# Kernel tuning notes

Hardware: AMD Instinct MI355X
Metric: run time of the kernel (lower is better)

## Reference

```python
import jax, jax.numpy as jnp
import numpy as np

H_S = 4
W_S = 4


def setup_inputs() -> dict:
    key = jax.random.key(0)
    k1, k2 = jax.random.split(key)
    x1 = jax.random.normal(k1, (8, 128, 96, 320), dtype=jnp.float32)
    x2 = jax.random.normal(k2, (8, 128, 96, 320), dtype=jnp.float32)
    return {"x1": x1, "x2": x2}


def reference(x1, x2):
    # torch F.pad p2d=(h_s,h_s,w_s,w_s) pads last dim (W) by h_s and H by w_s
    b, c, h, w = x1.shape
    padded = jnp.pad(x2, ((0, 0), (0, 0), (W_S, W_S), (H_S, H_S)))
    costs = []
    for y in range(2 * H_S + 1):
        for x in range(2 * W_S + 1):
            sl = padded[:, :, y:y + h, x:x + w]  # [B,C,H,W]
            costs.append(jnp.mean(x1 * sl, axis=1))  # [B,H,W]
    cost_vol = jnp.stack(costs, axis=1)  # [B,81,H,W]
    return jax.nn.leaky_relu(cost_vol, negative_slope=0.1)
```

## Files before the change

### kernel.cpp

```cpp
#include <hip/hip_runtime.h>
#include <stdint.h>


#define CCH   128
#define HH    96
#define WW    320
#define HWs   (HH * WW)
#define CHWs  (CCH * HWs)
#define ND    81

#define TH 4
#define WT 32
#define SW 40
#define SR 12
#define KC 32
#define KP 40
#define OP 132

typedef __attribute__((ext_vector_type(8))) short        short8;
typedef __attribute__((ext_vector_type(4))) float        floatx4;
typedef __attribute__((ext_vector_type(4))) unsigned int uint4v;

__device__ __forceinline__ unsigned int bf16rne(float f) {
  unsigned int u = __float_as_uint(f);
  return (u + 0x7fffu + ((u >> 16) & 1u)) >> 16;
}
__device__ __forceinline__ unsigned int pk2(float lo, float hi) {
  return bf16rne(lo) | (bf16rne(hi) << 16);
}

__global__ __launch_bounds__(512, 4) void cost_volume_kernel(
    const float* __restrict__ x1g, const float* __restrict__ x2g,
    float* __restrict__ out)
{
  extern __shared__ char smem[];
  short* x2s  = (short*)smem;
  float* obuf = (float*)smem;

  const int b  = blockIdx.x & 7;
  const int g  = blockIdx.x >> 3;
  const int hs = g % 24;
  const int ws = g / 24;
  const int h0 = hs * TH;
  const int W0 = ws * WT;

  const int t    = threadIdx.x;
  const int wave = t >> 6;
  const int lane = t & 63;
  const int hl   = wave >> 1;
  const int mt   = wave & 1;
  const int q    = lane >> 4;
  const int ln   = lane & 15;

  const float* x1b = x1g + (size_t)b * CHWs;
  const float* x2b = x2g + (size_t)b * CHWs;

  int x2_go[4], x2_lo[4];
#pragma unroll
  for (int s = 0; s < 4; ++s) {
    int u = t + s * 512;
    if (u < SR * SW * 4) {
      int j  = u % SW;
      int ro = u / SW;
      int o  = ro & 3;
      int r  = ro >> 2;
      int gr = h0 - 4 + r;
      int gc = W0 - 4 + j;
      x2_lo[s] = (r * SW + j) * KP + o * 8;
      x2_go[s] = (gr >= 0 && gr < HH && gc >= 0 && gc < WW)
                   ? (o * 8 * HWs + gr * WW + gc) : -1;
    } else { x2_lo[s] = -1; x2_go[s] = -1; }
  }
  const int x1off = (h0 + hl) * WW + W0 + mt * 16 + ln;

  floatx4 acc[9][2] = {};

  for (int kc = 0; kc < CCH / KC; ++kc) {
    const int cbase = kc * KC * HWs;

    const float* p1 = x1b + cbase + (size_t)q * 8 * HWs + x1off;
    float a0 = p1[0 * HWs], a1 = p1[1 * HWs], a2 = p1[2 * HWs], a3 = p1[3 * HWs];
    float a4 = p1[4 * HWs], a5 = p1[5 * HWs], a6 = p1[6 * HWs], a7 = p1[7 * HWs];

#pragma unroll
    for (int s = 0; s < 4; ++s) {
      if (x2_lo[s] >= 0) {
        unsigned int p01 = 0, p23 = 0, p45 = 0, p67 = 0;
        if (x2_go[s] >= 0) {
          const float* p = x2b + cbase + x2_go[s];
          float f0 = p[0 * HWs], f1 = p[1 * HWs], f2 = p[2 * HWs], f3 = p[3 * HWs];
          float f4 = p[4 * HWs], f5 = p[5 * HWs], f6 = p[6 * HWs], f7 = p[7 * HWs];
          p01 = pk2(f0, f1); p23 = pk2(f2, f3);
          p45 = pk2(f4, f5); p67 = pk2(f6, f7);
        }
        *(uint4v*)&x2s[x2_lo[s]] = (uint4v){p01, p23, p45, p67};
      }
    }

    short8 af;
    {
      uint4v av = (uint4v){pk2(a0, a1), pk2(a2, a3), pk2(a4, a5), pk2(a6, a7)};
      af = *(short8*)&av;
    }
    __syncthreads();

#pragma unroll
    for (int dyi = 0; dyi < 9; ++dyi) {
      const int r = hl + dyi;
#pragma unroll
      for (int jn = 0; jn < 2; ++jn) {
        int jc = (mt + jn) * 16 + ln;
        if (jc > SW - 1) jc = SW - 1;
        const short8 bf = *(const short8*)&x2s[(r * SW + jc) * KP + q * 8];
        acc[dyi][jn] = __builtin_amdgcn_mfma_f32_16x16x32_bf16(af, bf, acc[dyi][jn], 0, 0, 0);
      }
    }
    __syncthreads();
  }

  const size_t obase = (size_t)b * (ND * (size_t)HWs);
#pragma unroll
  for (int ph = 0; ph < 2; ++ph) {
    const int d0 = ph ? 5 : 0, d1 = ph ? 9 : 5;
#pragma unroll
    for (int dyi = 0; dyi < 9; ++dyi) {
      if (dyi < d0 || dyi >= d1) continue;
#pragma unroll
      for (int jn = 0; jn < 2; ++jn)
#pragma unroll
        for (int reg = 0; reg < 4; ++reg) {
          const int m   = q * 4 + reg;
          const int dxi = jn * 16 + ln - m;
          if (dxi >= 0 && dxi < 9) {
            float v = acc[dyi][jn][reg] * (1.0f / 128.0f);
            v = (v < 0.0f) ? 0.1f * v : v;
            obuf[((dyi - d0) * 9 + dxi) * OP + hl * WT + mt * 16 + m] = v;
          }
        }
    }
    __syncthreads();
    const int nd   = (d1 - d0) * 9;
    const int dbas = d0 * 9;
    for (int idx = t; idx < nd * TH * WT; idx += 512) {
      const int dl  = idx >> 7;
      const int rem = idx & 127;
      const int hh  = rem >> 5;
      const int wl  = rem & 31;
      out[obase + (size_t)(dbas + dl) * HWs + (h0 + hh) * WW + W0 + wl]
          = obuf[dl * OP + rem];
    }
    __syncthreads();
  }
}

extern "C" void kernel_launch(void* const* d_in, const int* in_sizes, int n_in,
                              void* d_out, int out_size, void* d_ws, size_t ws_size,
                              hipStream_t stream) {
  const float* x1 = (const float*)d_in[0];
  const float* x2 = (const float*)d_in[1];
  float* out = (float*)d_out;
  cost_volume_kernel<<<dim3(1920), dim3(512), 38400, stream>>>(x1, x2, out);
}
```

Before: 357.6 us.

## Split displacement rows across three blocks and stage x1 through LDS with float4 loads

Each tile is now split into three blocks, each covering three of the nine vertical displacements. This triples the grid and shrinks the accumulators from 18 to 6 per lane, so occupancy can rise. x1 and x2 are loaded as float4 along width, packed to bf16 and transposed into LDS, and the channel chunk doubles to 64 with two MFMA k-steps. The cost is that x1 and overlapping x2 rows are reloaded by three blocks, which adds global read traffic.

```diff
diff --git a/kernel.cpp b/kernel.cpp
--- a/kernel.cpp
+++ b/kernel.cpp
@@ -12,14 +12,16 @@
 #define TH 4
 #define WT 32
 #define SW 40
-#define SR 12
-#define KC 32
-#define KP 40
+#define SRr 6
+#define KC 64
+#define KP 68
 #define OP 132
+
+#define X2_LDS (SRr * SW * KP * 2)
+#define X1_LDS (TH * WT * KP * 2)
 
 typedef __attribute__((ext_vector_type(8))) short        short8;
 typedef __attribute__((ext_vector_type(4))) float        floatx4;
-typedef __attribute__((ext_vector_type(4))) unsigned int uint4v;
 
 __device__ __forceinline__ unsigned int bf16rne(float f) {
   unsigned int u = __float_as_uint(f);
@@ -29,20 +31,23 @@
   return bf16rne(lo) | (bf16rne(hi) << 16);
 }
 
-__global__ __launch_bounds__(512, 4) void cost_volume_kernel(
+__global__ __launch_bounds__(512, 6) void cost_volume_kernel(
     const float* __restrict__ x1g, const float* __restrict__ x2g,
     float* __restrict__ out)
 {
   extern __shared__ char smem[];
   short* x2s  = (short*)smem;
+  short* x1s  = (short*)(smem + X2_LDS);
   float* obuf = (float*)smem;
 
-  const int b  = blockIdx.x & 7;
-  const int g  = blockIdx.x >> 3;
-  const int hs = g % 24;
-  const int ws = g / 24;
-  const int h0 = hs * TH;
-  const int W0 = ws * WT;
+  const int b    = blockIdx.x & 7;
+  const int y    = blockIdx.x >> 3;
+  const int g3   = y % 3;
+  const int tile = y / 3;
+  const int hs   = tile % 24;
+  const int ws   = tile / 24;
+  const int h0   = hs * TH;
+  const int W0   = ws * WT;
 
   const int t    = threadIdx.x;
   const int wave = t >> 6;
@@ -59,97 +64,110 @@
 #pragma unroll
   for (int s = 0; s < 4; ++s) {
     int u = t + s * 512;
-    if (u < SR * SW * 4) {
-      int j  = u % SW;
-      int ro = u / SW;
-      int o  = ro & 3;
-      int r  = ro >> 2;
-      int gr = h0 - 4 + r;
-      int gc = W0 - 4 + j;
-      x2_lo[s] = (r * SW + j) * KP + o * 8;
-      x2_go[s] = (gr >= 0 && gr < HH && gc >= 0 && gc < WW)
-                   ? (o * 8 * HWs + gr * WW + gc) : -1;
+    if (u < SRr * 32 * 10) {
+      int wq  = u % 10;
+      int tmp = u / 10;
+      int cp  = tmp % 32;
+      int r   = tmp / 32;
+      int gr  = h0 + g3 * 3 - 4 + r;
+      int gc0 = W0 - 4 + wq * 4;
+      x2_lo[s] = (r * SW + wq * 4) * KP + cp * 2;
+      x2_go[s] = (gr >= 0 && gr < HH && gc0 >= 0 && gc0 <= WW - 4)
+                   ? (cp * 2 * HWs + gr * WW + gc0) : -1;
     } else { x2_lo[s] = -1; x2_go[s] = -1; }
   }
-  const int x1off = (h0 + hl) * WW + W0 + mt * 16 + ln;
+  int x1_go[2], x1_lo[2];
+#pragma unroll
+  for (int s = 0; s < 2; ++s) {
+    int u   = t + s * 512;
+    int wq  = u % 8;
+    int tmp = u / 8;
+    int cp  = tmp % 32;
+    int hr  = tmp / 32;
+    x1_lo[s] = (hr * WT + wq * 4) * KP + cp * 2;
+    x1_go[s] = cp * 2 * HWs + (h0 + hr) * WW + W0 + wq * 4;
+  }
 
-  floatx4 acc[9][2] = {};
+  floatx4 acc[3][2] = {};
 
   for (int kc = 0; kc < CCH / KC; ++kc) {
     const int cbase = kc * KC * HWs;
 
-    const float* p1 = x1b + cbase + (size_t)q * 8 * HWs + x1off;
-    float a0 = p1[0 * HWs], a1 = p1[1 * HWs], a2 = p1[2 * HWs], a3 = p1[3 * HWs];
-    float a4 = p1[4 * HWs], a5 = p1[5 * HWs], a6 = p1[6 * HWs], a7 = p1[7 * HWs];
-
 #pragma unroll
     for (int s = 0; s < 4; ++s) {
       if (x2_lo[s] >= 0) {
-        unsigned int p01 = 0, p23 = 0, p45 = 0, p67 = 0;
         if (x2_go[s] >= 0) {
-          const float* p = x2b + cbase + x2_go[s];
-          float f0 = p[0 * HWs], f1 = p[1 * HWs], f2 = p[2 * HWs], f3 = p[3 * HWs];
-          float f4 = p[4 * HWs], f5 = p[5 * HWs], f6 = p[6 * HWs], f7 = p[7 * HWs];
-          p01 = pk2(f0, f1); p23 = pk2(f2, f3);
-          p45 = pk2(f4, f5); p67 = pk2(f6, f7);
+          const float4 fa = *(const float4*)(x2b + cbase + x2_go[s]);
+          const float4 fb = *(const float4*)(x2b + cbase + x2_go[s] + HWs);
+          *(unsigned int*)&x2s[x2_lo[s] + 0 * KP] = pk2(fa.x, fb.x);
+          *(unsigned int*)&x2s[x2_lo[s] + 1 * KP] = pk2(fa.y, fb.y);
+          *(unsigned int*)&x2s[x2_lo[s] + 2 * KP] = pk2(fa.z, fb.z);
+          *(unsigned int*)&x2s[x2_lo[s] + 3 * KP] = pk2(fa.w, fb.w);
+        } else {
+          *(unsigned int*)&x2s[x2_lo[s] + 0 * KP] = 0u;
+          *(unsigned int*)&x2s[x2_lo[s] + 1 * KP] = 0u;
+          *(unsigned int*)&x2s[x2_lo[s] + 2 * KP] = 0u;
+          *(unsigned int*)&x2s[x2_lo[s] + 3 * KP] = 0u;
         }
-        *(uint4v*)&x2s[x2_lo[s]] = (uint4v){p01, p23, p45, p67};
       }
     }
-
-    short8 af;
-    {
-      uint4v av = (uint4v){pk2(a0, a1), pk2(a2, a3), pk2(a4, a5), pk2(a6, a7)};
-      af = *(short8*)&av;
+#pragma unroll
+    for (int s = 0; s < 2; ++s) {
+      const float4 fa = *(const float4*)(x1b + cbase + x1_go[s]);
+      const float4 fb = *(const float4*)(x1b + cbase + x1_go[s] + HWs);
+      *(unsigned int*)&x1s[x1_lo[s] + 0 * KP] = pk2(fa.x, fb.x);
+      *(unsigned int*)&x1s[x1_lo[s] + 1 * KP] = pk2(fa.y, fb.y);
+      *(unsigned int*)&x1s[x1_lo[s] + 2 * KP] = pk2(fa.z, fb.z);
+      *(unsigned int*)&x1s[x1_lo[s] + 3 * KP] = pk2(fa.w, fb.w);
     }
     __syncthreads();
 
 #pragma unroll
-    for (int dyi = 0; dyi < 9; ++dyi) {
-      const int r = hl + dyi;
+    for (int ks = 0; ks < 2; ++ks) {
+      const short8 af = *(const short8*)
+          &x1s[(hl * WT + mt * 16 + ln) * KP + ks * 32 + q * 8];
 #pragma unroll
-      for (int jn = 0; jn < 2; ++jn) {
-        int jc = (mt + jn) * 16 + ln;
-        if (jc > SW - 1) jc = SW - 1;
-        const short8 bf = *(const short8*)&x2s[(r * SW + jc) * KP + q * 8];
-        acc[dyi][jn] = __builtin_amdgcn_mfma_f32_16x16x32_bf16(af, bf, acc[dyi][jn], 0, 0, 0);
+      for (int dyl = 0; dyl < 3; ++dyl) {
+        const int r = hl + dyl;
+#pragma unroll
+        for (int jn = 0; jn < 2; ++jn) {
+          int jc = (mt + jn) * 16 + ln;
+          if (jc > SW - 1) jc = SW - 1;
+          const short8 bf = *(const short8*)
+              &x2s[(r * SW + jc) * KP + ks * 32 + q * 8];
+          acc[dyl][jn] = __builtin_amdgcn_mfma_f32_16x16x32_bf16(
+              af, bf, acc[dyl][jn], 0, 0, 0);
+        }
       }
     }
     __syncthreads();
   }
 
-  const size_t obase = (size_t)b * (ND * (size_t)HWs);
 #pragma unroll
-  for (int ph = 0; ph < 2; ++ph) {
-    const int d0 = ph ? 5 : 0, d1 = ph ? 9 : 5;
+  for (int dyl = 0; dyl < 3; ++dyl)
 #pragma unroll
-    for (int dyi = 0; dyi < 9; ++dyi) {
-      if (dyi < d0 || dyi >= d1) continue;
+    for (int jn = 0; jn < 2; ++jn)
 #pragma unroll
-      for (int jn = 0; jn < 2; ++jn)
-#pragma unroll
-        for (int reg = 0; reg < 4; ++reg) {
-          const int m   = q * 4 + reg;
-          const int dxi = jn * 16 + ln - m;
-          if (dxi >= 0 && dxi < 9) {
-            float v = acc[dyi][jn][reg] * (1.0f / 128.0f);
-            v = (v < 0.0f) ? 0.1f * v : v;
-            obuf[((dyi - d0) * 9 + dxi) * OP + hl * WT + mt * 16 + m] = v;
-          }
+      for (int reg = 0; reg < 4; ++reg) {
+        const int m   = q * 4 + reg;
+        const int dxi = jn * 16 + ln - m;
+        if (dxi >= 0 && dxi < 9) {
+          float v = acc[dyl][jn][reg] * (1.0f / 128.0f);
+          v = (v < 0.0f) ? 0.1f * v : v;
+          obuf[(dyl * 9 + dxi) * OP + hl * WT + mt * 16 + m] = v;
         }
-    }
-    __syncthreads();
-    const int nd   = (d1 - d0) * 9;
-    const int dbas = d0 * 9;
-    for (int idx = t; idx < nd * TH * WT; idx += 512) {
-      const int dl  = idx >> 7;
-      const int rem = idx & 127;
-      const int hh  = rem >> 5;
-      const int wl  = rem & 31;
-      out[obase + (size_t)(dbas + dl) * HWs + (h0 + hh) * WW + W0 + wl]
-          = obuf[dl * OP + rem];
-    }
-    __syncthreads();
+      }
+  __syncthreads();
+
+  const size_t obase = (size_t)b * (ND * (size_t)HWs)
+                     + (size_t)(g3 * 27) * HWs;
+  for (int idx = t; idx < 27 * TH * WT; idx += 512) {
+    const int dl  = idx >> 7;
+    const int rem = idx & 127;
+    const int hh  = rem >> 5;
+    const int wl  = rem & 31;
+    out[obase + (size_t)dl * HWs + (h0 + hh) * WW + W0 + wl]
+        = obuf[dl * OP + rem];
   }
 }
 
@@ -159,5 +177,5 @@
   const float* x1 = (const float*)d_in[0];
   const float* x2 = (const float*)d_in[1];
   float* out = (float*)d_out;
-  cost_volume_kernel<<<dim3(1920), dim3(512), 38400, stream>>>(x1, x2, out);
+  cost_volume_kernel<<<dim3(5760), dim3(512), X2_LDS + X1_LDS, stream>>>(x1, x2, out);
 }
```

New measurement: 425.3 us. 18.9% more time.
